# Optimization experiments

Measured on AMD Instinct MI355X. Metric: run time of the kernel, lower is better.

Reference implementation:

```python
import jax, jax.numpy as jnp
import numpy as np

DEPTH = 6
B, D, E, H = 8192, 256, 256, 50
N_INNER = (1 << (DEPTH - 1)) - 1   # 31
N_LEAF = 1 << (DEPTH - 1)          # 32


def setup_inputs() -> dict:
    key = jax.random.key(0)
    ks = jax.random.split(key, 16)
    g = lambda k, shape, fan: (jax.random.normal(k, shape, dtype=jnp.float32)
                               / jnp.sqrt(jnp.float32(fan)))
    return {
        "x": jax.random.normal(ks[0], (B, D), dtype=jnp.float32),
        "enc_W": g(ks[1], (4, E, E), E),
        "enc_b": jnp.zeros((4, E), jnp.float32),
        # inner nodes, stacked over N_INNER
        "in_W1": g(ks[2], (N_INNER, E, H), E),
        "in_b1": jnp.zeros((N_INNER, H), jnp.float32),
        "in_Ww": g(ks[3], (N_INNER, H, D), H),
        "in_bw": jnp.zeros((N_INNER, D), jnp.float32),
        "in_Wb": g(ks[4], (N_INNER, H), H),
        "in_bb": jnp.zeros((N_INNER,), jnp.float32),
        "in_Wbeta": g(ks[5], (N_INNER, H), H),
        "in_bbeta": jnp.zeros((N_INNER,), jnp.float32),
        # leaf models, stacked over N_LEAF
        "lf_W1": g(ks[6], (N_LEAF, E, E), E),
        "lf_b1": jnp.zeros((N_LEAF, E), jnp.float32),
        "lf_W2": g(ks[7], (N_LEAF, E), E),
        "lf_b2": jnp.zeros((N_LEAF,), jnp.float32),
    }


def reference(x, enc_W, enc_b, in_W1, in_b1, in_Ww, in_bw, in_Wb, in_bb,
              in_Wbeta, in_bbeta, lf_W1, lf_b1, lf_W2, lf_b2):
    batch = x.shape[0]
    # encoder: 4 relu Dense layers
    emb = x
    for i in range(4):
        emb = jax.nn.relu(emb @ enc_W[i] + enc_b[i])

    # all inner-node gates in one batched pass  -> pR: [N_INNER, B]
    h = jax.nn.relu(jnp.einsum('be,neh->nbh', emb, in_W1) + in_b1[:, None, :])
    w = jax.nn.softmax(jnp.einsum('nbh,nhd->nbd', h, in_Ww) + in_bw[:, None, :], axis=-1)
    b = jnp.einsum('nbh,nh->nb', h, in_Wb) + in_bb[:, None]
    beta = jnp.einsum('nbh,nh->nb', h, in_Wbeta) + in_bbeta[:, None]
    pR = jax.nn.sigmoid(beta * (jnp.einsum('nbd,bd->nb', w, x) + b))

    # all leaf MLPs in one batched pass  -> y_leaf: [N_LEAF, B]
    hl = jax.nn.relu(jnp.einsum('be,leh->lbh', emb, lf_W1) + lf_b1[:, None, :])
    y_leaf = jnp.einsum('lbh,lh->lb', hl, lf_W2) + lf_b2[:, None]

    # path probabilities (heap ordering; right child weighted by pR)
    prob = jnp.ones((batch, 1), dtype=x.dtype)
    idx = 0
    for level in range(DEPTH - 1):
        cnt = 1 << level
        p = pR[idx:idx + cnt].T                       # [B, cnt]
        prob = jnp.stack([prob * (1.0 - p), prob * p], axis=-1).reshape(batch, 2 * cnt)
        idx += cnt

    return jnp.sum(prob * y_leaf.T, axis=1, keepdims=True)  # [B, 1]
```

## Files before the change

kernel.cpp:

```cpp
#include <hip/hip_runtime.h>


#define B_ROWS 8192
#define HDIM 50
#define HPAD 64

typedef _Float16 f16;
typedef _Float16 f16x8 __attribute__((ext_vector_type(8)));
typedef _Float16 f16x4 __attribute__((ext_vector_type(4)));
typedef float f32x4 __attribute__((ext_vector_type(4)));

static __device__ __forceinline__ f32x4 mfma16(f16x8 a, f16x8 b, f32x4 c) {
  return __builtin_amdgcn_mfma_f32_16x16x32_f16(a, b, c, 0, 0, 0);
}

static __device__ __forceinline__ void gload16(const void* g, void* l) {
  __builtin_amdgcn_global_load_lds(
      (const __attribute__((address_space(1))) unsigned int*)g,
      (__attribute__((address_space(3))) unsigned int*)l, 16, 0, 0);
}

__global__ void k_cast_f16(const float* __restrict__ in, f16* __restrict__ out, int n4) {
  int i = blockIdx.x * blockDim.x + threadIdx.x;
  if (i < n4) {
    float4 v = reinterpret_cast<const float4*>(in)[i];
    f16x4 o = { (f16)v.x, (f16)v.y, (f16)v.z, (f16)v.w };
    reinterpret_cast<f16x4*>(out)[i] = o;
  }
}

__global__ void k_tcast(const float* __restrict__ in, f16* __restrict__ out,
                        int R, int C, int Rp, int Cp) {
  __shared__ float t[32][33];
  const int s = blockIdx.z;
  const int r0 = blockIdx.x * 32, c0 = blockIdx.y * 32;
  const int tx = threadIdx.x, ty = threadIdx.y;
  const float* ip = in + (size_t)s * R * C;
  f16* op = out + (size_t)s * Cp * Rp;
#pragma unroll
  for (int i = 0; i < 4; ++i) {
    int r = r0 + ty + 8 * i, c = c0 + tx;
    t[ty + 8 * i][tx] = (r < R && c < C) ? ip[(size_t)r * C + c] : 0.f;
  }
  __syncthreads();
#pragma unroll
  for (int i = 0; i < 4; ++i) {
    int c = c0 + ty + 8 * i, r = r0 + tx;
    if (c < Cp && r < Rp) op[(size_t)c * Rp + r] = (f16)t[tx][ty + 8 * i];
  }
}

__global__ __launch_bounds__(256) void k_enc4(const float* __restrict__ x,
    const f16* __restrict__ encWT, const float* __restrict__ enc_b,
    f16* __restrict__ emb) {
  __shared__ f16 act[2][32][264];
  __shared__ f16 Bt[256][72];
  const int tid = threadIdx.x;
  const int wave = tid >> 6, lane = tid & 63;
  const int grp = lane >> 4, lid = lane & 15;
  const int row0 = blockIdx.x * 32;
  const int sr = tid >> 3, sc = (tid & 7) * 8;

  {
    const int xr = tid >> 3, xc = (tid & 7) * 32;
    const float* src = x + (size_t)(row0 + xr) * 256 + xc;
#pragma unroll
    for (int j = 0; j < 4; ++j) {
      float4 a = ((const float4*)src)[2 * j];
      float4 b = ((const float4*)src)[2 * j + 1];
      f16x8 o = { (f16)a.x, (f16)a.y, (f16)a.z, (f16)a.w,
                  (f16)b.x, (f16)b.y, (f16)b.z, (f16)b.w };
      *(f16x8*)&act[0][xr][xc + 8 * j] = o;
    }
  }
  __syncthreads();

  for (int l = 0; l < 4; ++l) {
    const int cur = l & 1, nxt = cur ^ 1;
    f32x4 acc[2][4] = {};
    for (int kt = 0; kt < 4; ++kt) {
#pragma unroll
      for (int p = 0; p < 8; ++p)
        *(f16x8*)&Bt[p * 32 + sr][sc] =
            *(const f16x8*)&encWT[(size_t)l * 65536 + (size_t)(p * 32 + sr) * 256 + kt * 64 + sc];
      __syncthreads();
#pragma unroll
      for (int kk = 0; kk < 2; ++kk) {
        f16x8 af[2], bf[4];
#pragma unroll
        for (int m = 0; m < 2; ++m)
          af[m] = *(const f16x8*)&act[cur][m * 16 + lid][kt * 64 + kk * 32 + grp * 8];
#pragma unroll
        for (int n = 0; n < 4; ++n)
          bf[n] = *(const f16x8*)&Bt[wave * 64 + n * 16 + lid][kk * 32 + grp * 8];
#pragma unroll
        for (int m = 0; m < 2; ++m)
#pragma unroll
          for (int n = 0; n < 4; ++n) acc[m][n] = mfma16(af[m], bf[n], acc[m][n]);
      }
      __syncthreads();
    }
#pragma unroll
    for (int n = 0; n < 4; ++n) {
      const int col = wave * 64 + n * 16 + lid;
      const float bv = enc_b[l * 256 + col];
#pragma unroll
      for (int m = 0; m < 2; ++m)
#pragma unroll
        for (int r = 0; r < 4; ++r) {
          float v = acc[m][n][r] + bv;
          act[nxt][m * 16 + grp * 4 + r][col] = (f16)(v > 0.f ? v : 0.f);
        }
    }
    __syncthreads();
  }
  {
    const int xr = tid >> 3, xc = (tid & 7) * 32;
#pragma unroll
    for (int j = 0; j < 4; ++j)
      *(f16x8*)&emb[(size_t)(row0 + xr) * 256 + xc + 8 * j] =
          *(const f16x8*)&act[0][xr][xc + 8 * j];
  }
}

__global__ __launch_bounds__(256) void k_inner(const f16* __restrict__ emb,
    const f16* __restrict__ W1T_all, const float* __restrict__ b1_all,
    const f16* __restrict__ WwT_all, const f16* __restrict__ x_h,
    const float* __restrict__ bw_all, const float* __restrict__ Wb_all,
    const float* __restrict__ bb_all, const float* __restrict__ Wbeta_all,
    const float* __restrict__ bbeta_all, float* __restrict__ pR) {
  __shared__ f16 At[64][72];
  __shared__ f16 B1t[64][72];
  __shared__ f16 ht[64][72];
  __shared__ float red[4][64][2];
  __shared__ float red2[4][64][2];
  __shared__ float bbuf[64], betabuf[64];

  const int tid = threadIdx.x;
  const int wave = tid >> 6, lane = tid & 63;
  const int grp = lane >> 4, lid = lane & 15;
  const int row0 = blockIdx.x * 64;
  const int node = blockIdx.y;
  const f16* W1T = W1T_all + (size_t)node * HPAD * 256;
  const f16* WwT = WwT_all + (size_t)node * 256 * HPAD;

  f16x8 bwf[2][4];
#pragma unroll
  for (int kk = 0; kk < 2; ++kk)
#pragma unroll
    for (int lb = 0; lb < 4; ++lb)
      bwf[kk][lb] = *(const f16x8*)&WwT[(size_t)(wave * 64 + lb * 16 + lid) * HPAD + kk * 32 + grp * 8];

  const int ar = tid >> 2, ac = (tid & 3) * 16;
  const f16* Ag  = emb + (size_t)(row0 + ar) * 256 + ac;
  const f16* B1g = W1T + (size_t)ar * 256 + ac;
  f16x8 a0, a1, w0, w1;
  a0 = *(const f16x8*)(Ag + 0);  a1 = *(const f16x8*)(Ag + 8);
  w0 = *(const f16x8*)(B1g + 0); w1 = *(const f16x8*)(B1g + 8);

  f32x4 acc1t[4] = {};
  for (int kt = 0; kt < 4; ++kt) {
    *(f16x8*)&At[ar][ac] = a0;  *(f16x8*)&At[ar][ac + 8] = a1;
    *(f16x8*)&B1t[ar][ac] = w0; *(f16x8*)&B1t[ar][ac + 8] = w1;
    __syncthreads();
    if (kt < 3) {
      const int kb = (kt + 1) * 64;
      a0 = *(const f16x8*)(Ag + kb);  a1 = *(const f16x8*)(Ag + kb + 8);
      w0 = *(const f16x8*)(B1g + kb); w1 = *(const f16x8*)(B1g + kb + 8);
    }
#pragma unroll
    for (int kk = 0; kk < 2; ++kk) {
      f16x8 b1f = *(const f16x8*)&B1t[wave * 16 + lid][kk * 32 + grp * 8];
#pragma unroll
      for (int m = 0; m < 4; ++m) {
        f16x8 a1f = *(const f16x8*)&At[m * 16 + lid][kk * 32 + grp * 8];
        acc1t[m] = mfma16(b1f, a1f, acc1t[m]);
      }
    }
    __syncthreads();
  }
  {
    const int hc = wave * 16 + grp * 4;
    float bva[4];
#pragma unroll
    for (int r = 0; r < 4; ++r) {
      const int c = hc + r;
      bva[r] = (c < HDIM) ? b1_all[node * HDIM + c] : 0.f;
    }
#pragma unroll
    for (int m = 0; m < 4; ++m) {
      f16x4 hv;
#pragma unroll
      for (int r = 0; r < 4; ++r) {
        float v = acc1t[m][r] + bva[r];
        hv[r] = (f16)(v > 0.f ? v : 0.f);
      }
      *(f16x4*)&ht[m * 16 + lid][hc] = hv;
    }
  }
  __syncthreads();

  f16x4 xv[4][4];
#pragma unroll
  for (int lb = 0; lb < 4; ++lb)
#pragma unroll
    for (int bb = 0; bb < 4; ++bb)
      xv[lb][bb] = *(const f16x4*)&x_h[(size_t)(row0 + bb * 16 + lid) * 256 +
                                       wave * 64 + lb * 16 + grp * 4];

  {
    const int brow = tid & 63;
    const int q = (wave + (brow >> 3)) & 3;
    f16x8 h0 = *(const f16x8*)&ht[brow][q * 16];
    f16x8 h1 = *(const f16x8*)&ht[brow][q * 16 + 8];
    float sb = 0.f, sbt = 0.f;
#pragma unroll
    for (int j = 0; j < 8; ++j) {
      const int c = q * 16 + j;
      if (c < HDIM) {
        float hv = (float)h0[j];
        sb  += hv * Wb_all[node * HDIM + c];
        sbt += hv * Wbeta_all[node * HDIM + c];
      }
    }
#pragma unroll
    for (int j = 0; j < 8; ++j) {
      const int c = q * 16 + 8 + j;
      if (c < HDIM) {
        float hv = (float)h1[j];
        sb  += hv * Wb_all[node * HDIM + c];
        sbt += hv * Wbeta_all[node * HDIM + c];
      }
    }
    red2[wave][brow][0] = sb;
    red2[wave][brow][1] = sbt;
  }

  f32x4 acc2t[4][4] = {};
#pragma unroll
  for (int kk = 0; kk < 2; ++kk) {
    f16x8 afh[4];
#pragma unroll
    for (int bb = 0; bb < 4; ++bb)
      afh[bb] = *(const f16x8*)&ht[bb * 16 + lid][kk * 32 + grp * 8];
#pragma unroll
    for (int lb = 0; lb < 4; ++lb)
#pragma unroll
      for (int bb = 0; bb < 4; ++bb)
        acc2t[lb][bb] = mfma16(bwf[kk][lb], afh[bb], acc2t[lb][bb]);
  }
  __syncthreads();
  if (tid < 64) {
    bbuf[tid]    = red2[0][tid][0] + red2[1][tid][0] + red2[2][tid][0] + red2[3][tid][0]
                   + bb_all[node];
    betabuf[tid] = red2[0][tid][1] + red2[1][tid][1] + red2[2][tid][1] + red2[3][tid][1]
                   + bbeta_all[node];
  }

  float s[4] = {0.f, 0.f, 0.f, 0.f}, dt[4] = {0.f, 0.f, 0.f, 0.f};
#pragma unroll
  for (int lb = 0; lb < 4; ++lb) {
    float4 bwv = *(const float4*)&bw_all[node * 256 + wave * 64 + lb * 16 + grp * 4];
    float bwa[4] = {bwv.x, bwv.y, bwv.z, bwv.w};
#pragma unroll
    for (int bb = 0; bb < 4; ++bb)
#pragma unroll
      for (int r = 0; r < 4; ++r) {
        float e = __expf(acc2t[lb][bb][r] + bwa[r]);
        s[bb] += e;
        dt[bb] += e * (float)xv[lb][bb][r];
      }
  }
#pragma unroll
  for (int bb = 0; bb < 4; ++bb) {
    s[bb]  += __shfl_xor(s[bb], 16, 64);  s[bb]  += __shfl_xor(s[bb], 32, 64);
    dt[bb] += __shfl_xor(dt[bb], 16, 64); dt[bb] += __shfl_xor(dt[bb], 32, 64);
  }
  if (lane < 16)
#pragma unroll
    for (int bb = 0; bb < 4; ++bb) {
      red[wave][bb * 16 + lane][0] = s[bb];
      red[wave][bb * 16 + lane][1] = dt[bb];
    }
  __syncthreads();
  if (tid < 64) {
    float S  = red[0][tid][0] + red[1][tid][0] + red[2][tid][0] + red[3][tid][0];
    float DT = red[0][tid][1] + red[1][tid][1] + red[2][tid][1] + red[3][tid][1];
    float z = betabuf[tid] * (DT / S + bbuf[tid]);
    pR[(size_t)(row0 + tid) * 32 + node] = 1.f / (1.f + __expf(-z));
  }
}

__global__ __launch_bounds__(512) void k_leaf(const f16* __restrict__ emb,
    const f16* __restrict__ W1T_all, const float* __restrict__ b1_all,
    const float* __restrict__ W2_all, const float* __restrict__ b2_all,
    float* __restrict__ y_leaf) {
  __shared__ f16 Alds[128 * 64];
  __shared__ f16 Blds[256 * 64];
  __shared__ float red[4][128];
  const int tid = threadIdx.x;
  const int wave = tid >> 6, lane = tid & 63;
  const int wm = wave >> 2, wn = wave & 3;
  const int grp = lane >> 4, lid = lane & 15;
  const int row0 = blockIdx.x * 128;
  const int leaf = blockIdx.y;
  const f16* WT = W1T_all + (size_t)leaf * 65536;
  const float* b1 = b1_all + leaf * 256;
  const float* W2 = W2_all + leaf * 256;

  const int lrow = lane >> 3;
  const int sslot = (lane & 7) ^ lrow;

  f32x4 acc[4][4] = {};
  const int swzA = (lid & 7);
  for (int kt = 0; kt < 4; ++kt) {
#pragma unroll
    for (int r2 = 0; r2 < 2; ++r2) {
      const int arow = r2 * 64 + wave * 8 + lrow;
      gload16(emb + (size_t)(row0 + arow) * 256 + kt * 64 + sslot * 8,
              (char*)Alds + r2 * 8192 + wave * 1024);
    }
#pragma unroll
    for (int r4 = 0; r4 < 4; ++r4) {
      const int brow = r4 * 64 + wave * 8 + lrow;
      gload16(WT + (size_t)brow * 256 + kt * 64 + sslot * 8,
              (char*)Blds + r4 * 8192 + wave * 1024);
    }
    __syncthreads();
#pragma unroll
    for (int kk = 0; kk < 2; ++kk) {
      f16x8 af[4], bf[4];
#pragma unroll
      for (int rb = 0; rb < 4; ++rb) {
        const int row = wm * 64 + rb * 16 + lid;
        af[rb] = *(const f16x8*)((const char*)Alds + row * 128 +
                                 (((kk * 4 + grp) ^ swzA) << 4));
      }
#pragma unroll
      for (int cb = 0; cb < 4; ++cb) {
        const int row = wn * 64 + cb * 16 + lid;
        bf[cb] = *(const f16x8*)((const char*)Blds + row * 128 +
                                 (((kk * 4 + grp) ^ swzA) << 4));
      }
#pragma unroll
      for (int cb = 0; cb < 4; ++cb)
#pragma unroll
        for (int rb = 0; rb < 4; ++rb)
          acc[cb][rb] = mfma16(bf[cb], af[rb], acc[cb][rb]);
    }
    __syncthreads();
  }
  float b1a[4][4], w2a[4][4];
#pragma unroll
  for (int cb = 0; cb < 4; ++cb) {
    float4 t1 = *(const float4*)&b1[wn * 64 + cb * 16 + grp * 4];
    float4 t2 = *(const float4*)&W2[wn * 64 + cb * 16 + grp * 4];
    b1a[cb][0] = t1.x; b1a[cb][1] = t1.y; b1a[cb][2] = t1.z; b1a[cb][3] = t1.w;
    w2a[cb][0] = t2.x; w2a[cb][1] = t2.y; w2a[cb][2] = t2.z; w2a[cb][3] = t2.w;
  }
  float rs[4] = {0.f, 0.f, 0.f, 0.f};
#pragma unroll
  for (int cb = 0; cb < 4; ++cb)
#pragma unroll
    for (int rb = 0; rb < 4; ++rb)
#pragma unroll
      for (int r = 0; r < 4; ++r) {
        float v = acc[cb][rb][r] + b1a[cb][r];
        v = v > 0.f ? v : 0.f;
        rs[rb] += v * w2a[cb][r];
      }
#pragma unroll
  for (int rb = 0; rb < 4; ++rb) {
    rs[rb] += __shfl_xor(rs[rb], 16, 64);
    rs[rb] += __shfl_xor(rs[rb], 32, 64);
  }
  if (lane < 16)
#pragma unroll
    for (int rb = 0; rb < 4; ++rb)
      red[wn][wm * 64 + rb * 16 + lane] = rs[rb];
  __syncthreads();
  if (tid < 128) {
    float y = red[0][tid] + red[1][tid] + red[2][tid] + red[3][tid] + b2_all[leaf];
    y_leaf[(size_t)(row0 + tid) * 32 + leaf] = y;
  }
}

__global__ void k_combine(const float* __restrict__ pR, const float* __restrict__ y_leaf,
                          float* __restrict__ out) {
  const int b = blockIdx.x * 256 + threadIdx.x;
  float p[32], y[32];
  const float4* pp = (const float4*)(pR + (size_t)b * 32);
  const float4* yp = (const float4*)(y_leaf + (size_t)b * 32);
#pragma unroll
  for (int i = 0; i < 8; ++i) {
    float4 v = pp[i]; p[i*4] = v.x; p[i*4+1] = v.y; p[i*4+2] = v.z; p[i*4+3] = v.w;
    float4 w = yp[i]; y[i*4] = w.x; y[i*4+1] = w.y; y[i*4+2] = w.z; y[i*4+3] = w.w;
  }
  float o = 0.f;
#pragma unroll
  for (int l = 0; l < 32; ++l) {
    float pr = 1.f;
    int node = 0;
#pragma unroll
    for (int k = 0; k < 5; ++k) {
      const int bit = (l >> (4 - k)) & 1;
      const float pv = p[node];
      pr *= bit ? pv : (1.f - pv);
      node = 2 * node + 1 + bit;
    }
    o += pr * y[l];
  }
  out[b] = o;
}

extern "C" void kernel_launch(void* const* d_in, const int* in_sizes, int n_in,
                              void* d_out, int out_size, void* d_ws, size_t ws_size,
                              hipStream_t stream) {
  (void)in_sizes; (void)n_in; (void)out_size; (void)ws_size;
  const float* x        = (const float*)d_in[0];
  const float* enc_W    = (const float*)d_in[1];
  const float* enc_b    = (const float*)d_in[2];
  const float* in_W1    = (const float*)d_in[3];
  const float* in_b1    = (const float*)d_in[4];
  const float* in_Ww    = (const float*)d_in[5];
  const float* in_bw    = (const float*)d_in[6];
  const float* in_Wb    = (const float*)d_in[7];
  const float* in_bb    = (const float*)d_in[8];
  const float* in_Wbeta = (const float*)d_in[9];
  const float* in_bbeta = (const float*)d_in[10];
  const float* lf_W1    = (const float*)d_in[11];
  const float* lf_b1    = (const float*)d_in[12];
  const float* lf_W2    = (const float*)d_in[13];
  const float* lf_b2    = (const float*)d_in[14];
  float* out = (float*)d_out;

  char* ws = (char*)d_ws;
  f16* x_h     = (f16*)(ws);
  f16* emb     = (f16*)(ws + 4194304);
  f16* encWT   = (f16*)(ws + 8388608);
  f16* lfW1T   = (f16*)(ws + 8912896);
  f16* inW1T   = (f16*)(ws + 13107200);
  f16* inWwT   = (f16*)(ws + 14123008);
  float* pR    = (float*)(ws + 15138816);
  float* y_leaf= (float*)(ws + 16187392);

  dim3 tb(32, 8);
  hipLaunchKernelGGL(k_cast_f16, dim3(2048), dim3(256), 0, stream, x, x_h, B_ROWS * 256 / 4);
  hipLaunchKernelGGL(k_tcast, dim3(8, 8, 4),  tb, 0, stream, enc_W, encWT, 256, 256, 256, 256);
  hipLaunchKernelGGL(k_tcast, dim3(8, 8, 32), tb, 0, stream, lf_W1, lfW1T, 256, 256, 256, 256);
  hipLaunchKernelGGL(k_tcast, dim3(8, 2, 31), tb, 0, stream, in_W1, inW1T, 256, 50, 256, 64);
  hipLaunchKernelGGL(k_tcast, dim3(2, 8, 31), tb, 0, stream, in_Ww, inWwT, 50, 256, 64, 256);

  hipLaunchKernelGGL(k_enc4, dim3(256), dim3(256), 0, stream, x, encWT, enc_b, emb);
  hipLaunchKernelGGL(k_inner, dim3(128, 31), dim3(256), 0, stream, emb, inW1T, in_b1,
                     inWwT, x_h, in_bw, in_Wb, in_bb, in_Wbeta, in_bbeta, pR);
  hipLaunchKernelGGL(k_leaf, dim3(64, 32), dim3(512), 0, stream, emb, lfW1T, lf_b1, lf_W2, lf_b2, y_leaf);
  hipLaunchKernelGGL(k_combine, dim3(32), dim3(256), 0, stream, pR, y_leaf, out);
}
```

Before: 252.1 us.

## Restructure inner-node kernel so each wave handles one node over a shared emb tile

The inner-node kernel now loads a 64-row emb tile into LDS once per block and gives each of the four waves its own tree node. Before, each block covered one node and all waves split that node's work. Each wave computes the full hidden layer and softmax over all 256 outputs in chunks, streaming the W1 and Ww fragments straight from global memory with double buffering. This removes the cross-wave LDS reductions and most block barriers, and cuts redundant emb reads from 31 to 8 per row tile. The cost is more per-wave register pressure (launch bounds of 2) and uncoalesced global weight fragment loads. With 31 nodes, the wave assigned to node 31 idles after the load.

```diff
diff --git a/kernel.cpp b/kernel.cpp
--- a/kernel.cpp
+++ b/kernel.cpp
@@ -123,171 +123,147 @@
   }
 }
 
-__global__ __launch_bounds__(256) void k_inner(const f16* __restrict__ emb,
+__global__ __launch_bounds__(256, 2) void k_inner(const f16* __restrict__ emb,
     const f16* __restrict__ W1T_all, const float* __restrict__ b1_all,
     const f16* __restrict__ WwT_all, const f16* __restrict__ x_h,
     const float* __restrict__ bw_all, const float* __restrict__ Wb_all,
     const float* __restrict__ bb_all, const float* __restrict__ Wbeta_all,
     const float* __restrict__ bbeta_all, float* __restrict__ pR) {
-  __shared__ f16 At[64][72];
-  __shared__ f16 B1t[64][72];
-  __shared__ f16 ht[64][72];
-  __shared__ float red[4][64][2];
-  __shared__ float red2[4][64][2];
-  __shared__ float bbuf[64], betabuf[64];
+  __shared__ f16 et[64][264];
+  __shared__ f16 hbuf[4][64][72];
+  __shared__ float bbuf[4][64], betabuf[4][64];
 
   const int tid = threadIdx.x;
   const int wave = tid >> 6, lane = tid & 63;
   const int grp = lane >> 4, lid = lane & 15;
   const int row0 = blockIdx.x * 64;
-  const int node = blockIdx.y;
+  const int node = blockIdx.y * 4 + wave;
+
+  {
+    const int r = tid >> 2, cb = (tid & 3) * 64;
+#pragma unroll
+    for (int j = 0; j < 8; ++j)
+      *(f16x8*)&et[r][cb + 8 * j] =
+          *(const f16x8*)&emb[(size_t)(row0 + r) * 256 + cb + 8 * j];
+  }
+  __syncthreads();
+  if (node >= 31) return;
+
   const f16* W1T = W1T_all + (size_t)node * HPAD * 256;
   const f16* WwT = WwT_all + (size_t)node * 256 * HPAD;
 
-  f16x8 bwf[2][4];
-#pragma unroll
-  for (int kk = 0; kk < 2; ++kk)
-#pragma unroll
-    for (int lb = 0; lb < 4; ++lb)
-      bwf[kk][lb] = *(const f16x8*)&WwT[(size_t)(wave * 64 + lb * 16 + lid) * HPAD + kk * 32 + grp * 8];
-
-  const int ar = tid >> 2, ac = (tid & 3) * 16;
-  const f16* Ag  = emb + (size_t)(row0 + ar) * 256 + ac;
-  const f16* B1g = W1T + (size_t)ar * 256 + ac;
-  f16x8 a0, a1, w0, w1;
-  a0 = *(const f16x8*)(Ag + 0);  a1 = *(const f16x8*)(Ag + 8);
-  w0 = *(const f16x8*)(B1g + 0); w1 = *(const f16x8*)(B1g + 8);
-
-  f32x4 acc1t[4] = {};
-  for (int kt = 0; kt < 4; ++kt) {
-    *(f16x8*)&At[ar][ac] = a0;  *(f16x8*)&At[ar][ac + 8] = a1;
-    *(f16x8*)&B1t[ar][ac] = w0; *(f16x8*)&B1t[ar][ac + 8] = w1;
-    __syncthreads();
-    if (kt < 3) {
-      const int kb = (kt + 1) * 64;
-      a0 = *(const f16x8*)(Ag + kb);  a1 = *(const f16x8*)(Ag + kb + 8);
-      w0 = *(const f16x8*)(B1g + kb); w1 = *(const f16x8*)(B1g + kb + 8);
-    }
-#pragma unroll
-    for (int kk = 0; kk < 2; ++kk) {
-      f16x8 b1f = *(const f16x8*)&B1t[wave * 16 + lid][kk * 32 + grp * 8];
-#pragma unroll
-      for (int m = 0; m < 4; ++m) {
-        f16x8 a1f = *(const f16x8*)&At[m * 16 + lid][kk * 32 + grp * 8];
-        acc1t[m] = mfma16(b1f, a1f, acc1t[m]);
-      }
-    }
-    __syncthreads();
-  }
-  {
-    const int hc = wave * 16 + grp * 4;
+  f32x4 acc1[4][4] = {};
+  f16x8 wf[2][4];
+#pragma unroll
+  for (int h4 = 0; h4 < 4; ++h4)
+    wf[0][h4] = *(const f16x8*)&W1T[(size_t)(h4 * 16 + lid) * 256 + grp * 8];
+  for (int kt = 0; kt < 8; ++kt) {
+    const int cur = kt & 1, nxt = cur ^ 1;
+    if (kt < 7) {
+#pragma unroll
+      for (int h4 = 0; h4 < 4; ++h4)
+        wf[nxt][h4] = *(const f16x8*)&W1T[(size_t)(h4 * 16 + lid) * 256 +
+                                          (kt + 1) * 32 + grp * 8];
+    }
+    f16x8 af[4];
+#pragma unroll
+    for (int m = 0; m < 4; ++m)
+      af[m] = *(const f16x8*)&et[m * 16 + lid][kt * 32 + grp * 8];
+#pragma unroll
+    for (int h4 = 0; h4 < 4; ++h4)
+#pragma unroll
+      for (int m = 0; m < 4; ++m)
+        acc1[h4][m] = mfma16(wf[cur][h4], af[m], acc1[h4][m]);
+  }
+#pragma unroll
+  for (int h4 = 0; h4 < 4; ++h4) {
+    const int hc = h4 * 16 + grp * 4;
     float bva[4];
 #pragma unroll
-    for (int r = 0; r < 4; ++r) {
-      const int c = hc + r;
-      bva[r] = (c < HDIM) ? b1_all[node * HDIM + c] : 0.f;
-    }
+    for (int r = 0; r < 4; ++r)
+      bva[r] = (hc + r < HDIM) ? b1_all[node * HDIM + hc + r] : 0.f;
 #pragma unroll
     for (int m = 0; m < 4; ++m) {
       f16x4 hv;
 #pragma unroll
       for (int r = 0; r < 4; ++r) {
-        float v = acc1t[m][r] + bva[r];
+        float v = acc1[h4][m][r] + bva[r];
         hv[r] = (f16)(v > 0.f ? v : 0.f);
       }
-      *(f16x4*)&ht[m * 16 + lid][hc] = hv;
-    }
-  }
-  __syncthreads();
-
-  f16x4 xv[4][4];
-#pragma unroll
-  for (int lb = 0; lb < 4; ++lb)
-#pragma unroll
-    for (int bb = 0; bb < 4; ++bb)
-      xv[lb][bb] = *(const f16x4*)&x_h[(size_t)(row0 + bb * 16 + lid) * 256 +
-                                       wave * 64 + lb * 16 + grp * 4];
+      *(f16x4*)&hbuf[wave][m * 16 + lid][hc] = hv;
+    }
+  }
 
   {
-    const int brow = tid & 63;
-    const int q = (wave + (brow >> 3)) & 3;
-    f16x8 h0 = *(const f16x8*)&ht[brow][q * 16];
-    f16x8 h1 = *(const f16x8*)&ht[brow][q * 16 + 8];
     float sb = 0.f, sbt = 0.f;
 #pragma unroll
-    for (int j = 0; j < 8; ++j) {
-      const int c = q * 16 + j;
-      if (c < HDIM) {
-        float hv = (float)h0[j];
-        sb  += hv * Wb_all[node * HDIM + c];
-        sbt += hv * Wbeta_all[node * HDIM + c];
-      }
-    }
-#pragma unroll
-    for (int j = 0; j < 8; ++j) {
-      const int c = q * 16 + 8 + j;
-      if (c < HDIM) {
-        float hv = (float)h1[j];
-        sb  += hv * Wb_all[node * HDIM + c];
-        sbt += hv * Wbeta_all[node * HDIM + c];
-      }
-    }
-    red2[wave][brow][0] = sb;
-    red2[wave][brow][1] = sbt;
-  }
-
-  f32x4 acc2t[4][4] = {};
-#pragma unroll
-  for (int kk = 0; kk < 2; ++kk) {
-    f16x8 afh[4];
-#pragma unroll
-    for (int bb = 0; bb < 4; ++bb)
-      afh[bb] = *(const f16x8*)&ht[bb * 16 + lid][kk * 32 + grp * 8];
-#pragma unroll
-    for (int lb = 0; lb < 4; ++lb)
-#pragma unroll
-      for (int bb = 0; bb < 4; ++bb)
-        acc2t[lb][bb] = mfma16(bwf[kk][lb], afh[bb], acc2t[lb][bb]);
-  }
-  __syncthreads();
-  if (tid < 64) {
-    bbuf[tid]    = red2[0][tid][0] + red2[1][tid][0] + red2[2][tid][0] + red2[3][tid][0]
-                   + bb_all[node];
-    betabuf[tid] = red2[0][tid][1] + red2[1][tid][1] + red2[2][tid][1] + red2[3][tid][1]
-                   + bbeta_all[node];
+    for (int v8 = 0; v8 < 7; ++v8) {
+      f16x8 hv = *(const f16x8*)&hbuf[wave][lane][v8 * 8];
+#pragma unroll
+      for (int j = 0; j < 8; ++j) {
+        const int c = v8 * 8 + j;
+        if (c < HDIM) {
+          float hvf = (float)hv[j];
+          sb  += hvf * Wb_all[node * HDIM + c];
+          sbt += hvf * Wbeta_all[node * HDIM + c];
+        }
+      }
+    }
+    bbuf[wave][lane] = sb + bb_all[node];
+    betabuf[wave][lane] = sbt + bbeta_all[node];
   }
 
   float s[4] = {0.f, 0.f, 0.f, 0.f}, dt[4] = {0.f, 0.f, 0.f, 0.f};
-#pragma unroll
-  for (int lb = 0; lb < 4; ++lb) {
-    float4 bwv = *(const float4*)&bw_all[node * 256 + wave * 64 + lb * 16 + grp * 4];
-    float bwa[4] = {bwv.x, bwv.y, bwv.z, bwv.w};
-#pragma unroll
-    for (int bb = 0; bb < 4; ++bb)
-#pragma unroll
-      for (int r = 0; r < 4; ++r) {
-        float e = __expf(acc2t[lb][bb][r] + bwa[r]);
-        s[bb] += e;
-        dt[bb] += e * (float)xv[lb][bb][r];
-      }
-  }
-#pragma unroll
-  for (int bb = 0; bb < 4; ++bb) {
-    s[bb]  += __shfl_xor(s[bb], 16, 64);  s[bb]  += __shfl_xor(s[bb], 32, 64);
-    dt[bb] += __shfl_xor(dt[bb], 16, 64); dt[bb] += __shfl_xor(dt[bb], 32, 64);
-  }
-  if (lane < 16)
-#pragma unroll
-    for (int bb = 0; bb < 4; ++bb) {
-      red[wave][bb * 16 + lane][0] = s[bb];
-      red[wave][bb * 16 + lane][1] = dt[bb];
-    }
-  __syncthreads();
-  if (tid < 64) {
-    float S  = red[0][tid][0] + red[1][tid][0] + red[2][tid][0] + red[3][tid][0];
-    float DT = red[0][tid][1] + red[1][tid][1] + red[2][tid][1] + red[3][tid][1];
-    float z = betabuf[tid] * (DT / S + bbuf[tid]);
-    pR[(size_t)(row0 + tid) * 32 + node] = 1.f / (1.f + __expf(-z));
+  for (int c = 0; c < 4; ++c) {
+    f16x8 awf[2][4];
+#pragma unroll
+    for (int kk = 0; kk < 2; ++kk)
+#pragma unroll
+      for (int n4 = 0; n4 < 4; ++n4)
+        awf[kk][n4] = *(const f16x8*)&WwT[(size_t)(c * 64 + n4 * 16 + lid) * HPAD +
+                                          kk * 32 + grp * 8];
+    f32x4 acc2[4][4] = {};
+#pragma unroll
+    for (int kk = 0; kk < 2; ++kk) {
+      f16x8 hf[4];
+#pragma unroll
+      for (int m = 0; m < 4; ++m)
+        hf[m] = *(const f16x8*)&hbuf[wave][m * 16 + lid][kk * 32 + grp * 8];
+#pragma unroll
+      for (int n4 = 0; n4 < 4; ++n4)
+#pragma unroll
+        for (int m = 0; m < 4; ++m)
+          acc2[n4][m] = mfma16(awf[kk][n4], hf[m], acc2[n4][m]);
+    }
+#pragma unroll
+    for (int n4 = 0; n4 < 4; ++n4) {
+      float4 bwv = *(const float4*)&bw_all[node * 256 + c * 64 + n4 * 16 + grp * 4];
+      float bwa[4] = {bwv.x, bwv.y, bwv.z, bwv.w};
+#pragma unroll
+      for (int m = 0; m < 4; ++m) {
+        f16x4 xv = *(const f16x4*)&x_h[(size_t)(row0 + m * 16 + lid) * 256 +
+                                       c * 64 + n4 * 16 + grp * 4];
+#pragma unroll
+        for (int r = 0; r < 4; ++r) {
+          float e = __expf(acc2[n4][m][r] + bwa[r]);
+          s[m] += e;
+          dt[m] += e * (float)xv[r];
+        }
+      }
+    }
+  }
+#pragma unroll
+  for (int m = 0; m < 4; ++m) {
+    s[m]  += __shfl_xor(s[m], 16, 64);  s[m]  += __shfl_xor(s[m], 32, 64);
+    dt[m] += __shfl_xor(dt[m], 16, 64); dt[m] += __shfl_xor(dt[m], 32, 64);
+  }
+  if (grp == 0) {
+#pragma unroll
+    for (int m = 0; m < 4; ++m) {
+      const int row = m * 16 + lid;
+      float z = betabuf[wave][row] * (dt[m] / s[m] + bbuf[wave][row]);
+      pR[(size_t)(row0 + row) * 32 + node] = 1.f / (1.f + __expf(-z));
+    }
   }
 }
 
@@ -452,7 +428,7 @@
   hipLaunchKernelGGL(k_tcast, dim3(2, 8, 31), tb, 0, stream, in_Ww, inWwT, 50, 256, 64, 256);
 
   hipLaunchKernelGGL(k_enc4, dim3(256), dim3(256), 0, stream, x, encWT, enc_b, emb);
-  hipLaunchKernelGGL(k_inner, dim3(128, 31), dim3(256), 0, stream, emb, inW1T, in_b1,
+  hipLaunchKernelGGL(k_inner, dim3(128, 8), dim3(256), 0, stream, emb, inW1T, in_b1,
                      inWwT, x_h, in_bw, in_Wb, in_bb, in_Wbeta, in_bbeta, pR);
   hipLaunchKernelGGL(k_leaf, dim3(64, 32), dim3(512), 0, stream, emb, lfW1T, lf_b1, lf_W2, lf_b2, y_leaf);
   hipLaunchKernelGGL(k_combine, dim3(32), dim3(256), 0, stream, pR, y_leaf, out);
```

Measured after the change: 232.3 us. -7.9%, faster.
